# Optimization experiments

Hardware: AMD Instinct MI355X
Metric: run time of the kernel (lower is better)

Reference implementation:

```python
import jax, jax.numpy as jnp
import numpy as np

B, N, J = 8, 2048, 1024
QD, CD, H, D = 1024, 768, 16, 64
INNER = H * D


def setup_inputs() -> dict:
    key = jax.random.key(0)
    ks = jax.random.split(key, 7)
    s = 0.02
    return {
        "x": jax.random.normal(ks[0], (B, N, QD), jnp.float32),
        "context": jax.random.normal(ks[1], (B, J, CD), jnp.float32),
        "Wq": jax.random.normal(ks[2], (QD, INNER), jnp.float32) * s,
        "Wk": jax.random.normal(ks[3], (CD, INNER), jnp.float32) * s,
        "Wv": jax.random.normal(ks[4], (CD, INNER), jnp.float32) * s,
        "Wo": jax.random.normal(ks[5], (INNER, QD), jnp.float32) * s,
        "bo": jnp.zeros((QD,), jnp.float32),
    }


def reference(x, context, Wq, Wk, Wv, Wo, bo):
    scale = D ** (-0.5)
    # projections, then split heads: b n (h d) -> b h n d
    q = (x @ Wq).reshape(B, N, H, D).transpose(0, 2, 1, 3)
    k = (context @ Wk).reshape(B, J, H, D).transpose(0, 2, 1, 3)
    v = (context @ Wv).reshape(B, J, H, D).transpose(0, 2, 1, 3)
    sim = jnp.einsum("bhid,bhjd->bhij", q, k) * scale  # [B,H,N,J]
    attn = jax.nn.softmax(sim, axis=-1)
    out = jnp.einsum("bhij,bhjd->bhid", attn, v)  # [B,H,N,D]
    out = out.transpose(0, 2, 1, 3).reshape(B, N, INNER)
    return out @ Wo + bo
```

## Files before the change

### kernel.cpp

```cpp
#include <hip/hip_runtime.h>

#define B_     8
#define N_     2048
#define J_     1024
#define QD_    1024
#define CD_    768
#define H_     16
#define D_     64
#define INNER_ 1024

typedef __attribute__((ext_vector_type(8)))  __bf16 bf16x8;
typedef __attribute__((ext_vector_type(4)))  __bf16 bf16x4;
typedef __attribute__((ext_vector_type(4)))  float  f32x4;
typedef __attribute__((ext_vector_type(16))) float  f32x16;

__device__ __forceinline__ __bf16 to_bf16(float f) { return (__bf16)f; }

__device__ __forceinline__ unsigned pack2(float lo, float hi) {
    union { __bf16 h; unsigned short u; } a, b;
    a.h = (__bf16)lo; b.h = (__bf16)hi;
    return (unsigned)a.u | ((unsigned)b.u << 16);
}

__global__ __launch_bounds__(256)
void cvt_bf16_k(const float* __restrict__ s, __bf16* __restrict__ d, int n4)
{
    int i = blockIdx.x * 256 + threadIdx.x;
    if (i >= n4) return;
    float4 v = ((const float4*)s)[i];
    bf16x4 o;
    o[0] = (__bf16)v.x; o[1] = (__bf16)v.y; o[2] = (__bf16)v.z; o[3] = (__bf16)v.w;
    ((bf16x4*)d)[i] = o;
}

__global__ __launch_bounds__(256)
void transpose_bf16(const float* __restrict__ W, __bf16* __restrict__ Wt, int K, int N, float scale)
{
    __shared__ float tile[32][33];
    const int n0 = blockIdx.x * 32;
    const int k0 = blockIdx.y * 32;
    const int tx = threadIdx.x & 31;
    const int ty = threadIdx.x >> 5;
#pragma unroll
    for (int r = 0; r < 32; r += 8)
        tile[ty + r][tx] = W[(size_t)(k0 + ty + r) * N + n0 + tx];
    __syncthreads();
#pragma unroll
    for (int r = 0; r < 32; r += 8)
        Wt[(size_t)(n0 + ty + r) * K + k0 + tx] = to_bf16(tile[tx][ty + r] * scale);
}

template<int FINAL>
__global__ __launch_bounds__(256)
void gemm_bt(const __bf16* __restrict__ A, const __bf16* __restrict__ Bt,
             __bf16* __restrict__ Cb, __bf16* __restrict__ Cb2, float* __restrict__ Cf,
             const float* __restrict__ bias, int M, int N, int K)
{
    __shared__ __bf16 Asm[128 * 32];
    __shared__ __bf16 Bsm[128 * 32];

    const int tid = threadIdx.x;
    const int wid = tid >> 6;
    const int l   = tid & 63;
    const int lo  = l & 15, hi = l >> 4;

    const int nwg  = gridDim.x;
    const int work = ((int)blockIdx.x & 7) * (nwg >> 3) + ((int)blockIdx.x >> 3);
    const int gn   = N >> 7;
    const int m0   = (work / gn) * 128;
    const int n0   = (work % gn) * 128;

    const int wm  = (wid >> 1) * 64, wn = (wid & 1) * 64;

    f32x4 acc[4][4] = {};

    const int srow = (l >> 2);
    const int scol = (l & 3) * 8;

    for (int kt = 0; kt < K; kt += 32) {
#pragma unroll
        for (int i = 0; i < 2; ++i) {
            const int rbase = wid * 32 + i * 16;
            const __bf16* ga = A  + (size_t)(m0 + rbase + srow) * K + kt + scol;
            __builtin_amdgcn_global_load_lds((const __attribute__((address_space(1))) void*)ga,
                                             (__attribute__((address_space(3))) void*)&Asm[rbase * 32],
                                             16, 0, 0);
            const __bf16* gb = Bt + (size_t)(n0 + rbase + srow) * K + kt + scol;
            __builtin_amdgcn_global_load_lds((const __attribute__((address_space(1))) void*)gb,
                                             (__attribute__((address_space(3))) void*)&Bsm[rbase * 32],
                                             16, 0, 0);
        }
        __syncthreads();

        bf16x8 af[4], bfr[4];
#pragma unroll
        for (int i = 0; i < 4; ++i) {
            af[i]  = *(const bf16x8*)&Asm[(wm + i * 16 + lo) * 32 + hi * 8];
            bfr[i] = *(const bf16x8*)&Bsm[(wn + i * 16 + lo) * 32 + hi * 8];
        }
#pragma unroll
        for (int i = 0; i < 4; ++i)
#pragma unroll
            for (int j = 0; j < 4; ++j)
                acc[i][j] = __builtin_amdgcn_mfma_f32_16x16x32_bf16(af[i], bfr[j], acc[i][j], 0, 0, 0);
        __syncthreads();
    }

#pragma unroll
    for (int i = 0; i < 4; ++i) {
        const int row = m0 + wm + i * 16 + hi * 4;
#pragma unroll
        for (int j = 0; j < 4; ++j) {
            const int col = n0 + wn + j * 16 + lo;
            if (FINAL == 3) {
                if (col < 1024) {
#pragma unroll
                    for (int r = 0; r < 4; ++r)
                        Cb[(size_t)(row + r) * 1024 + col] = to_bf16(acc[i][j][r]);
                } else {
                    const int c2 = col - 1024;
                    const int head = c2 >> 6, d = c2 & 63;
                    const int bb = row >> 10, jj = row & 1023;
                    bf16x4 v4;
#pragma unroll
                    for (int r = 0; r < 4; ++r) v4[r] = to_bf16(acc[i][j][r]);
                    *(bf16x4*)&Cb2[(((size_t)(bb * 16 + head)) * 64 + d) * (size_t)J_ + jj] = v4;
                }
            } else {
#pragma unroll
                for (int r = 0; r < 4; ++r) {
                    if (FINAL == 1) Cf[(size_t)(row + r) * N + col] = acc[i][j][r] + bias[col];
                    else            Cb[(size_t)(row + r) * N + col] = to_bf16(acc[i][j][r]);
                }
            }
        }
    }
}

#define SEGE 544

__global__ __launch_bounds__(256, 3)
void attn2(const __bf16* __restrict__ Qb, const __bf16* __restrict__ Kb,
           const __bf16* __restrict__ Vt, __bf16* __restrict__ Ob)
{
    __shared__ __bf16 sK[2][8 * SEGE];
    __shared__ __bf16 sV[2][8 * SEGE];

    const int tid = threadIdx.x;
    const int wid = tid >> 6;
    const int l   = tid & 63;
    const int lq  = l & 31;
    const int hi  = l >> 5;

    const int blk  = blockIdx.x;
    const int work = (blk & 7) * 256 + (blk >> 3);
    const int qt = work & 15;
    const int h  = (work >> 4) & 15;
    const int b  = work >> 8;
    const int bh = b * H_ + h;

    bf16x8 qf[4];
    {
        const __bf16* qp = Qb + ((size_t)b * N_ + qt * 128 + wid * 32 + lq) * INNER_ + h * D_;
#pragma unroll
        for (int kc = 0; kc < 4; ++kc)
            qf[kc] = *(const bf16x8*)(qp + kc * 16 + hi * 8);
    }

    f32x16 accO[2] = {};
    float lsum = 0.f;

    const int srow = l >> 3, schk = l & 7;
    const __bf16* ksrc = Kb + ((size_t)b * J_ + wid * 8 + srow) * INNER_ + h * D_ + ((schk ^ srow) * 8);
    const __bf16* vsrc = Vt + ((size_t)bh * D_ + wid * 8 + srow) * J_ + ((schk ^ srow) * 8);

#define STAGE_T(bb, t) do { \
    _Pragma("unroll") \
    for (int c = 0; c < 2; ++c) { \
        __builtin_amdgcn_global_load_lds((const __attribute__((address_space(1))) void*)(ksrc + ((size_t)(t) * 64 + c * 32) * INNER_), \
            (__attribute__((address_space(3))) void*)(&sK[bb][(c * 4 + wid) * SEGE]), 16, 0, 0); \
        __builtin_amdgcn_global_load_lds((const __attribute__((address_space(1))) void*)(vsrc + (size_t)(c) * 32 * J_ + (t) * 64), \
            (__attribute__((address_space(3))) void*)(&sV[bb][(c * 4 + wid) * SEGE]), 16, 0, 0); \
    } } while (0)

    STAGE_T(0, 0);
    __syncthreads();

    for (int t = 0; t < J_ / 64; ++t) {
        const int bb = t & 1;
        if (t < J_ / 64 - 1) STAGE_T(bb ^ 1, t + 1);

        const __bf16* Ks = sK[bb];
        const __bf16* Vs = sV[bb];

#pragma unroll
        for (int jsub = 0; jsub < 2; ++jsub) {
            bf16x8 kf[4], vf[2][2];
            const int ksg = (jsub * 4 + (lq >> 3)) * SEGE + (lq & 7) * 64;
#pragma unroll
            for (int kc = 0; kc < 4; ++kc)
                kf[kc] = *(const bf16x8*)&Ks[ksg + (((kc * 2 + hi) ^ (lq & 7)) * 8)];
#pragma unroll
            for (int dt = 0; dt < 2; ++dt) {
                const int vsg = (dt * 4 + (lq >> 3)) * SEGE + (lq & 7) * 64;
#pragma unroll
                for (int k2 = 0; k2 < 2; ++k2)
                    vf[dt][k2] = *(const bf16x8*)&Vs[vsg + ((((jsub * 2 + k2) * 2 + hi) ^ (lq & 7)) * 8)];
            }

            f32x16 s = {};
            __builtin_amdgcn_s_setprio(1);
#pragma unroll
            for (int kc = 0; kc < 4; ++kc)
                s = __builtin_amdgcn_mfma_f32_32x32x16_bf16(kf[kc], qf[kc], s, 0, 0, 0);
            __builtin_amdgcn_s_setprio(0);

            float p[16];
#pragma unroll
            for (int r = 0; r < 16; ++r)
                p[r] = __builtin_amdgcn_exp2f(s[r]);
            {
                float t0 = (p[0] + p[1]) + (p[2] + p[3]);
                float t1 = (p[4] + p[5]) + (p[6] + p[7]);
                float t2 = (p[8] + p[9]) + (p[10] + p[11]);
                float t3 = (p[12] + p[13]) + (p[14] + p[15]);
                lsum += (t0 + t1) + (t2 + t3);
            }

#pragma unroll
            for (int k2 = 0; k2 < 2; ++k2) {
                unsigned a0 = pack2(p[k2 * 8 + 0], p[k2 * 8 + 1]);
                unsigned a1 = pack2(p[k2 * 8 + 2], p[k2 * 8 + 3]);
                unsigned b0 = pack2(p[k2 * 8 + 4], p[k2 * 8 + 5]);
                unsigned b1 = pack2(p[k2 * 8 + 6], p[k2 * 8 + 7]);
                unsigned sw0 = __shfl_xor(hi ? a0 : b0, 32);
                unsigned sw1 = __shfl_xor(hi ? a1 : b1, 32);
                union { unsigned u[4]; bf16x8 v; } pu;
                pu.u[0] = hi ? sw0 : a0;
                pu.u[1] = hi ? sw1 : a1;
                pu.u[2] = hi ? b0  : sw0;
                pu.u[3] = hi ? b1  : sw1;
                __builtin_amdgcn_s_setprio(1);
#pragma unroll
                for (int dt = 0; dt < 2; ++dt)
                    accO[dt] = __builtin_amdgcn_mfma_f32_32x32x16_bf16(vf[dt][k2], pu.v, accO[dt], 0, 0, 0);
                __builtin_amdgcn_s_setprio(0);
            }
        }
        __syncthreads();
    }
#undef STAGE_T

    {
        float lt = lsum + __shfl_xor(lsum, 32);
        float inv = 1.f / lt;
        __bf16* op = Ob + ((size_t)b * N_ + qt * 128 + wid * 32 + lq) * INNER_ + h * D_;
#pragma unroll
        for (int dt = 0; dt < 2; ++dt)
#pragma unroll
            for (int g = 0; g < 4; ++g) {
                bf16x4 v4;
#pragma unroll
                for (int e = 0; e < 4; ++e) v4[e] = to_bf16(accO[dt][g * 4 + e] * inv);
                *(bf16x4*)&op[dt * 32 + g * 8 + hi * 4] = v4;
            }
    }
}

extern "C" void kernel_launch(void* const* d_in, const int* in_sizes, int n_in,
                              void* d_out, int out_size, void* d_ws, size_t ws_size,
                              hipStream_t stream)
{
    const float* x   = (const float*)d_in[0];
    const float* ctx = (const float*)d_in[1];
    const float* Wq  = (const float*)d_in[2];
    const float* Wk  = (const float*)d_in[3];
    const float* Wv  = (const float*)d_in[4];
    const float* Wo  = (const float*)d_in[5];
    const float* bo  = (const float*)d_in[6];
    float* out = (float*)d_out;

    char* w = (char*)d_ws;
    auto take = [&](size_t bytes) { char* p = w; w += bytes; return p; };
    __bf16* xb  = (__bf16*)take((size_t)B_ * N_ * QD_ * 2);
    __bf16* cb  = (__bf16*)take((size_t)B_ * J_ * CD_ * 2);
    __bf16* wqt = (__bf16*)take((size_t)QD_ * INNER_ * 2);
    __bf16* wkt = (__bf16*)take((size_t)CD_ * INNER_ * 2);
    __bf16* wvt = (__bf16*)take((size_t)CD_ * INNER_ * 2);
    __bf16* wot = (__bf16*)take((size_t)INNER_ * QD_ * 2);
    __bf16* Qb  = (__bf16*)take((size_t)B_ * N_ * INNER_ * 2);
    __bf16* Kb  = (__bf16*)take((size_t)B_ * J_ * INNER_ * 2);
    __bf16* Vt  = (__bf16*)take((size_t)B_ * J_ * INNER_ * 2);
    __bf16* Ob  = xb;

    const float SCALE_Q = 0.125f * 1.44269504088896f;

    cvt_bf16_k<<<(B_ * N_ * QD_) / 1024, 256, 0, stream>>>(x,   xb, (B_ * N_ * QD_) / 4);
    cvt_bf16_k<<<(B_ * J_ * CD_) / 1024, 256, 0, stream>>>(ctx, cb, (B_ * J_ * CD_) / 4);

    transpose_bf16<<<dim3(INNER_ / 32, QD_ / 32), 256, 0, stream>>>(Wq, wqt, QD_, INNER_, SCALE_Q);
    transpose_bf16<<<dim3(INNER_ / 32, CD_ / 32), 256, 0, stream>>>(Wk, wkt, CD_, INNER_, 1.f);
    transpose_bf16<<<dim3(INNER_ / 32, CD_ / 32), 256, 0, stream>>>(Wv, wvt, CD_, INNER_, 1.f);
    transpose_bf16<<<dim3(QD_ / 32, INNER_ / 32), 256, 0, stream>>>(Wo, wot, INNER_, QD_, 1.f);

    gemm_bt<0><<<1024, 256, 0, stream>>>(xb, wqt, Qb, nullptr, nullptr, nullptr, B_ * N_, INNER_, QD_);
    gemm_bt<3><<<1024, 256, 0, stream>>>(cb, wkt, Kb, Vt, nullptr, nullptr, B_ * J_, 2 * INNER_, CD_);

    attn2<<<(N_ / 128) * H_ * B_, 256, 0, stream>>>(Qb, Kb, Vt, Ob);

    gemm_bt<1><<<1024, 256, 0, stream>>>(Ob, wot, nullptr, nullptr, out, bo, B_ * N_, QD_, INNER_);
}
```

Before: 290.3 us.

## Replace projection GEMMs with 256x256 double-buffered 8-wave pipelined kernel

Replaces the 128x128 single-buffered GEMM used for the Q, KV and output projections with a 256x256-tile, 512-thread kernel. Global-to-LDS loads are double-buffered and interleaved in quarters with MFMA blocks, using an XOR-swizzled LDS layout and setprio around the MFMA runs. The goal is to overlap memory with compute, cut LDS bank conflicts, and raise per-block data reuse. The larger tiles use 128 KB of LDS and more registers, and they launch only 256 blocks. The blockIdx swizzle for L2 locality is dropped.

Measured after the change: 266.5 us. 1.09x faster.

```diff
diff --git a/kernel.cpp b/kernel.cpp
--- a/kernel.cpp
+++ b/kernel.cpp
@@ -50,64 +50,124 @@
         Wt[(size_t)(n0 + ty + r) * K + k0 + tx] = to_bf16(tile[tx][ty + r] * scale);
 }
 
-template<int FINAL>
-__global__ __launch_bounds__(256)
-void gemm_bt(const __bf16* __restrict__ A, const __bf16* __restrict__ Bt,
-             __bf16* __restrict__ Cb, __bf16* __restrict__ Cb2, float* __restrict__ Cf,
-             const float* __restrict__ bias, int M, int N, int K)
-{
-    __shared__ __bf16 Asm[128 * 32];
-    __shared__ __bf16 Bsm[128 * 32];
+template<int FINAL, int KDIM>
+__global__ __launch_bounds__(512, 2)
+void gemm8(const __bf16* __restrict__ A, const __bf16* __restrict__ Bt,
+           __bf16* __restrict__ Cb, __bf16* __restrict__ Cb2, float* __restrict__ Cf,
+           const float* __restrict__ bias, int N)
+{
+    constexpr int NIT = KDIM / 64;
+    __shared__ __bf16 sA[2][16384];
+    __shared__ __bf16 sB[2][16384];
 
     const int tid = threadIdx.x;
     const int wid = tid >> 6;
     const int l   = tid & 63;
-    const int lo  = l & 15, hi = l >> 4;
-
-    const int nwg  = gridDim.x;
-    const int work = ((int)blockIdx.x & 7) * (nwg >> 3) + ((int)blockIdx.x >> 3);
-    const int gn   = N >> 7;
-    const int m0   = (work / gn) * 128;
-    const int n0   = (work % gn) * 128;
-
-    const int wm  = (wid >> 1) * 64, wn = (wid & 1) * 64;
-
-    f32x4 acc[4][4] = {};
-
-    const int srow = (l >> 2);
-    const int scol = (l & 3) * 8;
-
-    for (int kt = 0; kt < K; kt += 32) {
-#pragma unroll
-        for (int i = 0; i < 2; ++i) {
-            const int rbase = wid * 32 + i * 16;
-            const __bf16* ga = A  + (size_t)(m0 + rbase + srow) * K + kt + scol;
-            __builtin_amdgcn_global_load_lds((const __attribute__((address_space(1))) void*)ga,
-                                             (__attribute__((address_space(3))) void*)&Asm[rbase * 32],
-                                             16, 0, 0);
-            const __bf16* gb = Bt + (size_t)(n0 + rbase + srow) * K + kt + scol;
-            __builtin_amdgcn_global_load_lds((const __attribute__((address_space(1))) void*)gb,
-                                             (__attribute__((address_space(3))) void*)&Bsm[rbase * 32],
-                                             16, 0, 0);
-        }
-        __syncthreads();
-
-        bf16x8 af[4], bfr[4];
-#pragma unroll
-        for (int i = 0; i < 4; ++i) {
-            af[i]  = *(const bf16x8*)&Asm[(wm + i * 16 + lo) * 32 + hi * 8];
-            bfr[i] = *(const bf16x8*)&Bsm[(wn + i * 16 + lo) * 32 + hi * 8];
-        }
-#pragma unroll
-        for (int i = 0; i < 4; ++i)
-#pragma unroll
-            for (int j = 0; j < 4; ++j)
-                acc[i][j] = __builtin_amdgcn_mfma_f32_16x16x32_bf16(af[i], bfr[j], acc[i][j], 0, 0, 0);
-        __syncthreads();
-    }
-
-#pragma unroll
-    for (int i = 0; i < 4; ++i) {
+    const int lo  = l & 15, hi = (l >> 4) & 3;
+
+    const int gn = N >> 8;
+    const int m0 = ((int)blockIdx.x / gn) * 256;
+    const int n0 = ((int)blockIdx.x % gn) * 256;
+
+    const int wm  = (wid >> 2) * 128, wn = (wid & 3) * 64;
+    const int wmr = (wid >> 2) * 8,   bnr = (wid & 3) * 4;
+
+    int rOff[2], cOff[2], dOff[2];
+#pragma unroll
+    for (int n = 0; n < 2; ++n) {
+        const int s = n * 8 + wid;
+        rOff[n] = (s >> 1) * 16 + (l >> 2);
+        cOff[n] = (s & 1) * 32 + (((l & 3) * 8) ^ (((l >> 5) & 1) * 16));
+        dOff[n] = n * 4096 + wid * 512;
+    }
+
+    const int inner = lo * 32 + ((hi * 8) ^ ((lo >> 3) * 16));
+
+    f32x4 acc[8][4] = {};
+    bf16x8 af[4][2], bfr[4][2];
+
+#define STAGE8(nb, h, kt) do { \
+    _Pragma("unroll") \
+    for (int n = 0; n < 2; ++n) { \
+        const __bf16* gp = ((h) < 2 ? A + (size_t)(m0 + ((h) & 1) * 128 + rOff[n]) * KDIM \
+                                    : Bt + (size_t)(n0 + ((h) & 1) * 128 + rOff[n]) * KDIM) \
+                           + (kt) + cOff[n]; \
+        __bf16* dp = ((h) < 2 ? &sA[nb][((h) & 1) * 8192 + dOff[n]] \
+                              : &sB[nb][((h) & 1) * 8192 + dOff[n]]); \
+        __builtin_amdgcn_global_load_lds((const __attribute__((address_space(1))) void*)gp, \
+                                         (__attribute__((address_space(3))) void*)dp, 16, 0, 0); \
+    } } while (0)
+
+#define RD_A(x0, cnt, nb) do { \
+    _Pragma("unroll") \
+    for (int x = 0; x < (cnt); ++x) \
+        _Pragma("unroll") \
+        for (int kk = 0; kk < 2; ++kk) \
+            af[x][kk] = *(const bf16x8*)&sA[nb][((wmr + (x0) + x) * 2 + kk) * 512 + inner]; \
+    } while (0)
+
+#define RD_B(j0, cnt, nb) do { \
+    _Pragma("unroll") \
+    for (int j = 0; j < (cnt); ++j) \
+        _Pragma("unroll") \
+        for (int kk = 0; kk < 2; ++kk) \
+            bfr[(j0) + j][kk] = *(const bf16x8*)&sB[nb][((bnr + (j0) + j) * 2 + kk) * 512 + inner]; \
+    } while (0)
+
+#define MMQ(mh, nh) do { \
+    __builtin_amdgcn_s_setprio(1); \
+    _Pragma("unroll") \
+    for (int x = 0; x < 4; ++x) \
+        _Pragma("unroll") \
+        for (int j = 0; j < 2; ++j) \
+            _Pragma("unroll") \
+            for (int kk = 0; kk < 2; ++kk) \
+                acc[(mh) * 4 + x][(nh) * 2 + j] = __builtin_amdgcn_mfma_f32_16x16x32_bf16( \
+                    af[x][kk], bfr[(nh) * 2 + j][kk], acc[(mh) * 4 + x][(nh) * 2 + j], 0, 0, 0); \
+    __builtin_amdgcn_s_setprio(0); \
+    } while (0)
+
+#define BARR() do { __builtin_amdgcn_s_barrier(); \
+    asm volatile("" ::: "memory"); __builtin_amdgcn_sched_barrier(0); } while (0)
+
+#pragma unroll
+    for (int h = 0; h < 4; ++h) STAGE8(0, h, 0);
+
+    for (int it = 0; it < NIT; ++it) {
+        const int nb = it & 1, nbn = nb ^ 1;
+        const int ktn = (it + 1) * 64;
+        const bool notlast = (it < NIT - 1);
+
+        if (notlast) STAGE8(nbn, 0, ktn);
+        if (notlast) asm volatile("s_waitcnt vmcnt(2)" ::: "memory");
+        else         asm volatile("s_waitcnt vmcnt(0)" ::: "memory");
+        BARR();
+        RD_A(0, 4, nb); RD_B(0, 2, nb);
+        MMQ(0, 0);
+        BARR();
+        if (notlast) STAGE8(nbn, 1, ktn);
+        BARR();
+        RD_B(2, 2, nb);
+        MMQ(0, 1);
+        BARR();
+        if (notlast) STAGE8(nbn, 2, ktn);
+        BARR();
+        RD_A(4, 4, nb);
+        MMQ(1, 0);
+        BARR();
+        if (notlast) STAGE8(nbn, 3, ktn);
+        BARR();
+        MMQ(1, 1);
+        BARR();
+    }
+#undef STAGE8
+#undef RD_A
+#undef RD_B
+#undef MMQ
+#undef BARR
+
+#pragma unroll
+    for (int i = 0; i < 8; ++i) {
         const int row = m0 + wm + i * 16 + hi * 4;
 #pragma unroll
         for (int j = 0; j < 4; ++j) {
@@ -303,10 +363,10 @@
     transpose_bf16<<<dim3(INNER_ / 32, CD_ / 32), 256, 0, stream>>>(Wv, wvt, CD_, INNER_, 1.f);
     transpose_bf16<<<dim3(QD_ / 32, INNER_ / 32), 256, 0, stream>>>(Wo, wot, INNER_, QD_, 1.f);
 
-    gemm_bt<0><<<1024, 256, 0, stream>>>(xb, wqt, Qb, nullptr, nullptr, nullptr, B_ * N_, INNER_, QD_);
-    gemm_bt<3><<<1024, 256, 0, stream>>>(cb, wkt, Kb, Vt, nullptr, nullptr, B_ * J_, 2 * INNER_, CD_);
+    gemm8<0, QD_><<<256, 512, 0, stream>>>(xb, wqt, Qb, nullptr, nullptr, nullptr, INNER_);
+    gemm8<3, CD_><<<256, 512, 0, stream>>>(cb, wkt, Kb, Vt, nullptr, nullptr, 2 * INNER_);
 
     attn2<<<(N_ / 128) * H_ * B_, 256, 0, stream>>>(Qb, Kb, Vt, Ob);
 
-    gemm_bt<1><<<1024, 256, 0, stream>>>(Ob, wot, nullptr, nullptr, out, bo, B_ * N_, QD_, INNER_);
-}
+    gemm8<1, INNER_><<<256, 512, 0, stream>>>(Ob, wot, nullptr, nullptr, out, bo, QD_);
+}
```
